# Optimization experiments

Hardware: AMD Instinct MI355X
Metric: run time of the kernel (lower is better)

Reference implementation:

```python
import jax, jax.numpy as jnp
import numpy as np

B, T, D = 2, 1024, 2048
H, KV, DH = 16, 4, 128
REP = H // KV
LAMBDA_INIT = 0.8 - 0.6 * float(np.exp(-0.3 * 1))  # layer_idx=2
ROPE_BASE = 10000.0
GN_EPS = 1e-5


def _rope(x, pos):
    # x: (B, h, T, DH), pos: (T,) int
    inv = 1.0 / (ROPE_BASE ** (jnp.arange(0, DH, 2, dtype=jnp.float32) / DH))
    freqs = pos.astype(jnp.float32)[:, None] * inv[None, :]          # (T, DH/2)
    cos = jnp.cos(freqs)[None, None, :, :].astype(x.dtype)
    sin = jnp.sin(freqs)[None, None, :, :].astype(x.dtype)
    x1, x2 = x[..., ::2], x[..., 1::2]
    o1 = x1 * cos - x2 * sin
    o2 = x1 * sin + x2 * cos
    return jnp.stack([o1, o2], axis=-1).reshape(x.shape)


def setup_inputs() -> dict:
    key = jax.random.key(0)
    ks = jax.random.split(key, 10)
    s = 0.02
    return {
        "x": jax.random.normal(ks[0], (B, T, D), jnp.float32),
        "Wq": jax.random.normal(ks[1], (2 * H * DH, D), jnp.float32) * s,
        "Wk": jax.random.normal(ks[2], (2 * KV * DH, D), jnp.float32) * s,
        "Wv": jax.random.normal(ks[3], (2 * KV * DH, D), jnp.float32) * s,
        "Wo": jax.random.normal(ks[4], (D, 2 * H * DH), jnp.float32) * s,
        "lambda_q1": jax.random.normal(ks[5], (DH,), jnp.float32) * 0.1,
        "lambda_k1": jax.random.normal(ks[6], (DH,), jnp.float32) * 0.1,
        "lambda_q2": jax.random.normal(ks[7], (DH,), jnp.float32) * 0.1,
        "lambda_k2": jax.random.normal(ks[8], (DH,), jnp.float32) * 0.1,
        "gn_weight": jnp.ones((2 * H * DH,), jnp.float32),
        "gn_bias": jnp.zeros((2 * H * DH,), jnp.float32),
        "pos": jnp.arange(T, dtype=jnp.int64 if jax.config.jax_enable_x64 else jnp.int32),
    }


def reference(x, Wq, Wk, Wv, Wo, lambda_q1, lambda_k1, lambda_q2, lambda_k2, gn_weight, gn_bias, pos):
    b, t, _ = x.shape
    # projections
    q = (x @ Wq.T).reshape(b, t, H, 2, DH)        # two query streams per head
    k = (x @ Wk.T).reshape(b, t, KV, 2, DH)       # two key streams per kv-head
    v = (x @ Wv.T).reshape(b, t, KV, 2 * DH)      # single value, 2*Dh per kv-head
    q1 = q[..., 0, :].transpose(0, 2, 1, 3)       # (B,H,T,DH)
    q2 = q[..., 1, :].transpose(0, 2, 1, 3)
    k1 = k[..., 0, :].transpose(0, 2, 1, 3)       # (B,KV,T,DH)
    k2 = k[..., 1, :].transpose(0, 2, 1, 3)
    v = v.transpose(0, 2, 1, 3)                   # (B,KV,T,2DH)
    # RoPE on all Q/K streams
    q1, q2 = _rope(q1, pos), _rope(q2, pos)
    k1, k2 = _rope(k1, pos), _rope(k2, pos)
    # GQA repeat kv heads
    k1 = jnp.repeat(k1, REP, axis=1)
    k2 = jnp.repeat(k2, REP, axis=1)
    vr = jnp.repeat(v, REP, axis=1)               # (B,H,T,2DH)
    scale = DH ** -0.5
    neg = jnp.asarray(-jnp.inf, x.dtype)
    causal = jnp.tril(jnp.ones((t, t), bool))
    s1 = jnp.einsum("bhqd,bhkd->bhqk", q1, k1) * scale
    s2 = jnp.einsum("bhqd,bhkd->bhqk", q2, k2) * scale
    a1 = jax.nn.softmax(jnp.where(causal, s1, neg), axis=-1)
    a2 = jax.nn.softmax(jnp.where(causal, s2, neg), axis=-1)
    lam = (jnp.exp(jnp.sum(lambda_q1 * lambda_k1))
           - jnp.exp(jnp.sum(lambda_q2 * lambda_k2))
           + LAMBDA_INIT)
    attn = a1 - lam * a2
    out = jnp.einsum("bhqk,bhkd->bhqd", attn, vr)  # (B,H,T,2DH)
    # GroupNorm: num_groups=H over 2*H*DH channels == per-head norm over 2*DH
    o = out.transpose(0, 2, 1, 3)                  # (B,T,H,2DH)
    mu = jnp.mean(o, axis=-1, keepdims=True)
    var = jnp.var(o, axis=-1, keepdims=True)
    o = (o - mu) * jax.lax.rsqrt(var + GN_EPS)
    o = o * gn_weight.reshape(H, 2 * DH) + gn_bias.reshape(H, 2 * DH)
    o = o * (1.0 - LAMBDA_INIT)
    o = o.reshape(b, t, 2 * H * DH)
    return o @ Wo.T
```

## Files before the change

kernel.cpp:

```cpp
#include <hip/hip_runtime.h>
#include <hip/hip_bf16.h>

#define BB 2
#define TT 1024
#define DD 2048
#define NH 16
#define NKV 4
#define DHD 128
#define DVV 256

#define LAMBDA_INIT 0.35550906759096927f
#define ONE_MINUS_LI 0.6444909324090307f
#define QSCALE (0.08838834764831845f * 1.4426950408889634f)

typedef __attribute__((ext_vector_type(8))) short bf16x8;
typedef __attribute__((ext_vector_type(4))) float f32x4;

static __device__ __forceinline__ short f2bf_s(float x) {
    __hip_bfloat16 h = __float2bfloat16(x);
    return __builtin_bit_cast(short, h);
}
static __device__ __forceinline__ float bfu2f(unsigned short u) {
    union { float f; unsigned int u32; } x;
    x.u32 = ((unsigned int)u) << 16;
    return x.f;
}

#define GLOAD_LDS16(g, l)                                                      \
    __builtin_amdgcn_global_load_lds(                                          \
        (const __attribute__((address_space(1))) unsigned int*)(g),            \
        (__attribute__((address_space(3))) unsigned int*)(l), 16, 0, 0)

__global__ void cast_bf16(const float* __restrict__ in, __hip_bfloat16* __restrict__ out, int n4) {
    int i = blockIdx.x * blockDim.x + threadIdx.x;
    if (i >= n4) return;
    const float4 v = reinterpret_cast<const float4*>(in)[i];
    union { ushort4 u; __hip_bfloat16 b[4]; } o;
    o.b[0] = __float2bfloat16(v.x);
    o.b[1] = __float2bfloat16(v.y);
    o.b[2] = __float2bfloat16(v.z);
    o.b[3] = __float2bfloat16(v.w);
    reinterpret_cast<ushort4*>(out)[i] = o.u;
}

__global__ __launch_bounds__(256) void gemm128(const __hip_bfloat16* __restrict__ A,
                                               const __hip_bfloat16* __restrict__ Bm,
                                               float* __restrict__ C,
                                               int M, int N, int K) {
    __shared__ ushort As[128 * 32];
    __shared__ ushort Bs[128 * 32];
    const int tid = threadIdx.x;
    const int lane = tid & 63, wid = tid >> 6;
    const int lo = lane & 15, hi = lane >> 4;
    const int wr = wid >> 1, wc = wid & 1;
    const int m0 = blockIdx.y * 128, n0 = blockIdx.x * 128;

    const int srow = tid >> 2;
    const int scol = (tid & 3) << 3;

    const ushort* gA = (const ushort*)A;
    const ushort* gB = (const ushort*)Bm;

    f32x4 acc[4][4];
#pragma unroll
    for (int mi = 0; mi < 4; ++mi)
#pragma unroll
        for (int ni = 0; ni < 4; ++ni) acc[mi][ni] = (f32x4){0.f, 0.f, 0.f, 0.f};

    for (int k0 = 0; k0 < K; k0 += 32) {
        __syncthreads();
#pragma unroll
        for (int i = 0; i < 2; ++i) {
            GLOAD_LDS16(gA + (size_t)(m0 + i * 64 + srow) * K + k0 + scol,
                        &As[(i * 256 + wid * 64) * 8]);
            GLOAD_LDS16(gB + (size_t)(n0 + i * 64 + srow) * K + k0 + scol,
                        &Bs[(i * 256 + wid * 64) * 8]);
        }
        __syncthreads();

        bf16x8 af[4], bfr[4];
#pragma unroll
        for (int mi = 0; mi < 4; ++mi)
            af[mi] = *reinterpret_cast<const bf16x8*>(&As[(wr * 64 + mi * 16 + lo) * 32 + hi * 8]);
#pragma unroll
        for (int ni = 0; ni < 4; ++ni)
            bfr[ni] = *reinterpret_cast<const bf16x8*>(&Bs[(wc * 64 + ni * 16 + lo) * 32 + hi * 8]);
        __builtin_amdgcn_s_setprio(1);
#pragma unroll
        for (int mi = 0; mi < 4; ++mi)
#pragma unroll
            for (int ni = 0; ni < 4; ++ni)
                acc[mi][ni] = __builtin_amdgcn_mfma_f32_16x16x32_bf16(af[mi], bfr[ni], acc[mi][ni], 0, 0, 0);
        __builtin_amdgcn_s_setprio(0);
    }
#pragma unroll
    for (int mi = 0; mi < 4; ++mi)
#pragma unroll
        for (int ni = 0; ni < 4; ++ni)
#pragma unroll
            for (int r = 0; r < 4; ++r)
                C[(size_t)(m0 + wr * 64 + mi * 16 + hi * 4 + r) * N + (n0 + wc * 64 + ni * 16 + lo)] =
                    acc[mi][ni][r];
}

__global__ void rope_qk(const float* __restrict__ in, int stride, int col_base, int nheads, int hshift,
                        const int* __restrict__ pos, __hip_bfloat16* __restrict__ out, float scale) {
    int idx = blockIdx.x * blockDim.x + threadIdx.x;
    int total = BB * TT * nheads * 2 * 64;
    if (idx >= total) return;
    int d2 = idx & 63;
    int rest = idx >> 6;
    int e = rest & 1;
    int rest2 = rest >> 1;
    int head = rest2 & (nheads - 1);
    int bt = rest2 >> hshift;
    int t = bt & (TT - 1);
    int b = bt >> 10;

    const float* src = in + (size_t)bt * stride + col_base + head * 256 + e * 128 + 2 * d2;
    float x1 = src[0], x2 = src[1];
    float inv = expf(-(float)d2 * (2.0f / 128.0f) * 9.210340371976184f);
    float fr = (float)pos[t] * inv;
    float sn, cs;
    sincosf(fr, &sn, &cs);
    float o1 = (x1 * cs - x2 * sn) * scale;
    float o2 = (x1 * sn + x2 * cs) * scale;
    __hip_bfloat16* dst = out + ((((size_t)e * BB + b) * nheads + head) * TT + t) * DHD + 2 * d2;
    dst[0] = __float2bfloat16(o1);
    dst[1] = __float2bfloat16(o2);
}

__global__ void vtrans(const float* __restrict__ in, __hip_bfloat16* __restrict__ out) {
    int idx = blockIdx.x * blockDim.x + threadIdx.x;
    int total = BB * NKV * DVV * TT;
    if (idx >= total) return;
    int t = idx & (TT - 1);
    int rest = idx >> 10;
    int dv = rest & 255;
    int rest2 = rest >> 8;
    int kvi = rest2 & 3;
    int b = rest2 >> 2;
    out[idx] = __float2bfloat16(in[(size_t)(b * TT + t) * 6144 + 5120 + kvi * 256 + dv]);
}

__global__ void lam_k(const float* __restrict__ lq1, const float* __restrict__ lk1,
                      const float* __restrict__ lq2, const float* __restrict__ lk2,
                      float* __restrict__ lam) {
    int l = threadIdx.x;
    float s1 = lq1[l] * lk1[l] + lq1[l + 64] * lk1[l + 64];
    float s2 = lq2[l] * lk2[l] + lq2[l + 64] * lk2[l + 64];
#pragma unroll
    for (int mm = 1; mm < 64; mm <<= 1) {
        s1 += __shfl_xor(s1, mm, 64);
        s2 += __shfl_xor(s2, mm, 64);
    }
    if (l == 0) lam[0] = expf(s1) - expf(s2) + LAMBDA_INIT;
}

__global__ __launch_bounds__(256) void attn_fused(const __hip_bfloat16* __restrict__ qb,
                                                  const __hip_bfloat16* __restrict__ kb,
                                                  const __hip_bfloat16* __restrict__ vtb,
                                                  __hip_bfloat16* __restrict__ Obuf) {
    const int tid = threadIdx.x;
    const int wid = tid >> 6;
    const int lane = tid & 63;
    const int lo = lane & 15, hi = lane >> 4;
    const int qt = (int)gridDim.x - 1 - blockIdx.x;
    const int bh = blockIdx.y;
    const int e = blockIdx.z;
    const int b = bh >> 4, h = bh & 15;
    const int kv = h >> 2;

    const ushort* qp = (const ushort*)qb + (((size_t)e * BB + b) * NH + h) * (size_t)TT * DHD;
    const ushort* kp = (const ushort*)kb + (((size_t)e * BB + b) * NKV + kv) * (size_t)TT * DHD;
    const ushort* vp = (const ushort*)vtb + ((size_t)b * NKV + kv) * (size_t)DVV * TT;

    const int q0 = qt * 64 + wid * 16;

    __shared__ ushort Ks[64 * 128];
    __shared__ ushort Vs[256 * 64];

    bf16x8 qf[4];
#pragma unroll
    for (int kk = 0; kk < 4; ++kk)
        qf[kk] = *reinterpret_cast<const bf16x8*>(qp + (size_t)(q0 + lo) * DHD + kk * 32 + hi * 8);

    f32x4 O[16];
#pragma unroll
    for (int nc = 0; nc < 16; ++nc) O[nc] = (f32x4){0.f, 0.f, 0.f, 0.f};
    float m = -3e38f, l = 0.f;

    const int nkt = qt + 1;
    for (int kt = 0; kt < nkt; ++kt) {
        const int kbase = kt * 64;
#pragma unroll
        for (int p2 = 0; p2 < 4; ++p2) {
            const int idx = p2 * 256 + tid;
            const int row = idx >> 4, c = idx & 15;
            const int cp = c ^ ((row & 3) | ((row >> 1) & 4));
            GLOAD_LDS16(kp + (((size_t)(kbase + row)) << 7) + (cp << 3), &Ks[idx << 3]);
        }
#pragma unroll
        for (int p2 = 0; p2 < 8; ++p2) {
            const int idx = p2 * 256 + tid;
            const int dv = idx >> 3, c = idx & 7;
            const int cp = c ^ (dv & 7);
            GLOAD_LDS16(vp + (size_t)dv * TT + kbase + (cp << 3), &Vs[idx << 3]);
        }
        __syncthreads();

        f32x4 s[4];
#pragma unroll
        for (int n = 0; n < 4; ++n) s[n] = (f32x4){0.f, 0.f, 0.f, 0.f};
        __builtin_amdgcn_s_setprio(1);
#pragma unroll
        for (int n = 0; n < 4; ++n) {
            const int R = ((n >> 1) << 5) + ((lo >> 2) << 3) + ((n & 1) << 2) + (lo & 3);
            const int swz = ((R & 3) | ((R >> 1) & 4)) << 4;
#pragma unroll
            for (int kk = 0; kk < 4; ++kk) {
                bf16x8 kf = *reinterpret_cast<const bf16x8*>(
                    (const char*)Ks + R * 256 + ((kk * 64 + hi * 16) ^ swz));
                s[n] = __builtin_amdgcn_mfma_f32_16x16x32_bf16(kf, qf[kk], s[n], 0, 0, 0);
            }
        }
        __builtin_amdgcn_s_setprio(0);

        if (kt == nkt - 1) {
#pragma unroll
            for (int n = 0; n < 4; ++n) {
                const int kb0 = kbase + ((n >> 1) << 5) + ((n & 1) << 2) + hi * 8;
#pragma unroll
                for (int r = 0; r < 4; ++r)
                    if (kb0 + r > q0 + lo) s[n][r] = -3e38f;
            }
        }
        float tm = s[0][0];
#pragma unroll
        for (int n = 0; n < 4; ++n)
#pragma unroll
            for (int r = 0; r < 4; ++r) tm = fmaxf(tm, s[n][r]);
        tm = fmaxf(tm, __shfl_xor(tm, 16, 64));
        tm = fmaxf(tm, __shfl_xor(tm, 32, 64));
        if (!__all(tm <= m + 11.f)) {
            const float mn = fmaxf(m, tm);
            const float resc = __builtin_amdgcn_exp2f(m - mn);
            m = mn;
            l *= resc;
            float ro[4];
#pragma unroll
            for (int r = 0; r < 4; ++r) ro[r] = __shfl(resc, hi * 4 + r, 64);
#pragma unroll
            for (int nc = 0; nc < 16; ++nc)
#pragma unroll
                for (int r = 0; r < 4; ++r) O[nc][r] *= ro[r];
        }
        float rs = 0.f;
#pragma unroll
        for (int n = 0; n < 4; ++n)
#pragma unroll
            for (int r = 0; r < 4; ++r) {
                const float p = __builtin_amdgcn_exp2f(s[n][r] - m);
                s[n][r] = p;
                rs += p;
            }
        rs += __shfl_xor(rs, 16, 64);
        rs += __shfl_xor(rs, 32, 64);
        l += rs;
        bf16x8 pf[2];
#pragma unroll
        for (int n = 0; n < 4; ++n)
#pragma unroll
            for (int r = 0; r < 4; ++r) pf[n >> 1][(n & 1) * 4 + r] = f2bf_s(s[n][r]);
        __builtin_amdgcn_s_setprio(1);
#pragma unroll
        for (int nc = 0; nc < 16; ++nc) {
            const int vrow = (nc * 16 + lo) * 128;
            const int vswz = (lo & 7) << 4;
#pragma unroll
            for (int ks = 0; ks < 2; ++ks) {
                bf16x8 vf = *reinterpret_cast<const bf16x8*>(
                    (const char*)Vs + vrow + ((ks * 64 + hi * 16) ^ vswz));
                O[nc] = __builtin_amdgcn_mfma_f32_16x16x32_bf16(pf[ks], vf, O[nc], 0, 0, 0);
            }
        }
        __builtin_amdgcn_s_setprio(0);
        __syncthreads();
    }
    const float invl = 1.0f / l;
    float io[4];
#pragma unroll
    for (int r = 0; r < 4; ++r) io[r] = __shfl(invl, hi * 4 + r, 64);
    ushort* op = (ushort*)Obuf + (((size_t)e * BB + b) * NH + h) * (size_t)TT * DVV;
#pragma unroll
    for (int nc = 0; nc < 16; ++nc)
#pragma unroll
        for (int r = 0; r < 4; ++r)
            op[(size_t)(q0 + hi * 4 + r) * DVV + nc * 16 + lo] = (ushort)f2bf_s(O[nc][r] * io[r]);
}

__global__ __launch_bounds__(256) void gn_combine(const __hip_bfloat16* __restrict__ Obuf,
                                                  const float* __restrict__ lamp,
                                                  const float* __restrict__ gw, const float* __restrict__ gb,
                                                  __hip_bfloat16* __restrict__ obf) {
    const int wid = threadIdx.x >> 6, lane = threadIdx.x & 63;
    const int rid = blockIdx.x * 4 + wid;
    const int t = rid & (TT - 1);
    const int h = (rid >> 10) & 15;
    const int b = rid >> 14;
    const float lam = lamp[0];
    const size_t E = (size_t)BB * NH * TT * DVV;
    const ushort* o1p = (const ushort*)Obuf + (size_t)rid * DVV + lane * 4;
    const ushort4 u1 = *reinterpret_cast<const ushort4*>(o1p);
    const ushort4 u2 = *reinterpret_cast<const ushort4*>(o1p + E);
    float val[4];
    val[0] = bfu2f(u1.x) - lam * bfu2f(u2.x);
    val[1] = bfu2f(u1.y) - lam * bfu2f(u2.y);
    val[2] = bfu2f(u1.z) - lam * bfu2f(u2.z);
    val[3] = bfu2f(u1.w) - lam * bfu2f(u2.w);
    float sum = val[0] + val[1] + val[2] + val[3];
    float ss = val[0] * val[0] + val[1] * val[1] + val[2] * val[2] + val[3] * val[3];
#pragma unroll
    for (int mm = 1; mm < 64; mm <<= 1) {
        sum += __shfl_xor(sum, mm, 64);
        ss += __shfl_xor(ss, mm, 64);
    }
    const float mean = sum * (1.0f / 256.0f);
    const float var = ss * (1.0f / 256.0f) - mean * mean;
    const float rs = rsqrtf(var + 1e-5f);
    const int c = h * 256 + lane * 4;
    const float4 gwv = *reinterpret_cast<const float4*>(gw + c);
    const float4 gbv = *reinterpret_cast<const float4*>(gb + c);
    union { ushort4 u; short s[4]; } o;
    o.s[0] = f2bf_s(((val[0] - mean) * rs * gwv.x + gbv.x) * ONE_MINUS_LI);
    o.s[1] = f2bf_s(((val[1] - mean) * rs * gwv.y + gbv.y) * ONE_MINUS_LI);
    o.s[2] = f2bf_s(((val[2] - mean) * rs * gwv.z + gbv.z) * ONE_MINUS_LI);
    o.s[3] = f2bf_s(((val[3] - mean) * rs * gwv.w + gbv.w) * ONE_MINUS_LI);
    const int bt = b * TT + t;
    *reinterpret_cast<ushort4*>((ushort*)obf + (size_t)bt * 4096 + c) = o.u;
}

extern "C" void kernel_launch(void* const* d_in, const int* in_sizes, int n_in,
                              void* d_out, int out_size, void* d_ws, size_t ws_size,
                              hipStream_t stream) {
    const float* x = (const float*)d_in[0];
    const float* Wq = (const float*)d_in[1];
    const float* Wk = (const float*)d_in[2];
    const float* Wv = (const float*)d_in[3];
    const float* Wo = (const float*)d_in[4];
    const float* lq1 = (const float*)d_in[5];
    const float* lk1 = (const float*)d_in[6];
    const float* lq2 = (const float*)d_in[7];
    const float* lk2 = (const float*)d_in[8];
    const float* gw = (const float*)d_in[9];
    const float* gb = (const float*)d_in[10];
    const int* pos = (const int*)d_in[11];

    char* ws = (char*)d_ws;
    const size_t oXB = 0;
    const size_t oWQKV = 8388608;
    const size_t oWO = 33554432;
    const size_t oQKVF = 50331648;
    const size_t oOB = 50331648;
    const size_t oLAM = 83886080;
    const size_t oQB = 100663296;
    const size_t oKB = 117440512;
    const size_t oVT = 121634816;
    const size_t oON = 125829120;

    auto bfp = [&](size_t off) { return (__hip_bfloat16*)(ws + off); };
    auto fp = [&](size_t off) { return (float*)(ws + off); };

    int n;
    n = BB * TT * DD / 4;
    cast_bf16<<<dim3((n + 255) / 256), 256, 0, stream>>>(x, bfp(oXB), n);
    n = 4096 * 2048 / 4;
    cast_bf16<<<dim3((n + 255) / 256), 256, 0, stream>>>(Wq, bfp(oWQKV), n);
    n = 1024 * 2048 / 4;
    cast_bf16<<<dim3((n + 255) / 256), 256, 0, stream>>>(Wk, bfp(oWQKV + (size_t)4096 * 2048 * 2), n);
    cast_bf16<<<dim3((n + 255) / 256), 256, 0, stream>>>(Wv, bfp(oWQKV + (size_t)5120 * 2048 * 2), n);
    n = 2048 * 4096 / 4;
    cast_bf16<<<dim3((n + 255) / 256), 256, 0, stream>>>(Wo, bfp(oWO), n);

    gemm128<<<dim3(6144 / 128, 2048 / 128), 256, 0, stream>>>(bfp(oXB), bfp(oWQKV), fp(oQKVF), 2048, 6144, 2048);

    n = BB * TT * NH * 2 * 64;
    rope_qk<<<dim3((n + 255) / 256), 256, 0, stream>>>(fp(oQKVF), 6144, 0, NH, 4, pos, bfp(oQB), QSCALE);
    n = BB * TT * NKV * 2 * 64;
    rope_qk<<<dim3((n + 255) / 256), 256, 0, stream>>>(fp(oQKVF), 6144, 4096, NKV, 2, pos, bfp(oKB), 1.0f);
    n = BB * NKV * DVV * TT;
    vtrans<<<dim3((n + 255) / 256), 256, 0, stream>>>(fp(oQKVF), bfp(oVT));

    lam_k<<<dim3(1), 64, 0, stream>>>(lq1, lk1, lq2, lk2, fp(oLAM));

    attn_fused<<<dim3(TT / 64, BB * NH, 2), 256, 0, stream>>>(bfp(oQB), bfp(oKB), bfp(oVT), bfp(oOB));

    gn_combine<<<dim3(BB * NH * TT / 4), 256, 0, stream>>>(bfp(oOB), fp(oLAM), gw, gb, bfp(oON));

    gemm128<<<dim3(2048 / 128, 2048 / 128), 256, 0, stream>>>(bfp(oON), bfp(oWO), (float*)d_out, 2048, 2048, 4096);
}
```

Before: 484.4 us.

## Double-buffer GEMM LDS, split-K output projection, tile V transpose through LDS

The GEMM now keeps two LDS buffers, issuing the next K-tile's global-to-LDS loads before computing on the current one, so each iteration needs one barrier instead of two. The output projection is split along K into two slices written to a scratch partial buffer, then summed by a new addf4 kernel; this doubles the block count for a grid that otherwise fills the CUs only once, at the cost of extra partial-sum traffic and a launch. The V transpose now goes through a padded LDS tile so both the reads and the writes to global memory are coalesced. The s_setprio hints are removed.

```diff
diff --git a/kernel.cpp b/kernel.cpp
--- a/kernel.cpp
+++ b/kernel.cpp
@@ -43,23 +43,35 @@
     reinterpret_cast<ushort4*>(out)[i] = o.u;
 }
 
-__global__ __launch_bounds__(256) void gemm128(const __hip_bfloat16* __restrict__ A,
-                                               const __hip_bfloat16* __restrict__ Bm,
-                                               float* __restrict__ C,
-                                               int M, int N, int K) {
-    __shared__ ushort As[128 * 32];
-    __shared__ ushort Bs[128 * 32];
+__global__ __launch_bounds__(256) void gemm128_db(const __hip_bfloat16* __restrict__ A,
+                                                  const __hip_bfloat16* __restrict__ Bm,
+                                                  float* __restrict__ C,
+                                                  int M, int N, int sK, int kLen) {
+    __shared__ ushort As[2][128 * 32];
+    __shared__ ushort Bs[2][128 * 32];
     const int tid = threadIdx.x;
     const int lane = tid & 63, wid = tid >> 6;
     const int lo = lane & 15, hi = lane >> 4;
     const int wr = wid >> 1, wc = wid & 1;
     const int m0 = blockIdx.y * 128, n0 = blockIdx.x * 128;
-
-    const int srow = tid >> 2;
-    const int scol = (tid & 3) << 3;
+    const int kOff = blockIdx.z * kLen;
 
     const ushort* gA = (const ushort*)A;
     const ushort* gB = (const ushort*)Bm;
+    C += (size_t)blockIdx.z * M * N;
+
+    const int c0row = tid >> 2;
+    const int c0col = (tid & 3) << 3;
+
+    auto STAGE = [&](int buf, int kg) {
+#pragma unroll
+        for (int q = 0; q < 2; ++q) {
+            const int row = q * 64 + c0row;
+            const int idx = q * 256 + tid;
+            GLOAD_LDS16(gA + (size_t)(m0 + row) * sK + kg + c0col, &As[buf][idx << 3]);
+            GLOAD_LDS16(gB + (size_t)(n0 + row) * sK + kg + c0col, &Bs[buf][idx << 3]);
+        }
+    };
 
     f32x4 acc[4][4];
 #pragma unroll
@@ -67,31 +79,25 @@
 #pragma unroll
         for (int ni = 0; ni < 4; ++ni) acc[mi][ni] = (f32x4){0.f, 0.f, 0.f, 0.f};
 
-    for (int k0 = 0; k0 < K; k0 += 32) {
+    STAGE(0, kOff);
+    const int nt = kLen >> 5;
+    for (int t = 0; t < nt; ++t) {
         __syncthreads();
-#pragma unroll
-        for (int i = 0; i < 2; ++i) {
-            GLOAD_LDS16(gA + (size_t)(m0 + i * 64 + srow) * K + k0 + scol,
-                        &As[(i * 256 + wid * 64) * 8]);
-            GLOAD_LDS16(gB + (size_t)(n0 + i * 64 + srow) * K + k0 + scol,
-                        &Bs[(i * 256 + wid * 64) * 8]);
-        }
-        __syncthreads();
-
+        if (t + 1 < nt) STAGE((t + 1) & 1, kOff + ((t + 1) << 5));
+        const ushort* as = &As[t & 1][0];
+        const ushort* bs = &Bs[t & 1][0];
         bf16x8 af[4], bfr[4];
 #pragma unroll
         for (int mi = 0; mi < 4; ++mi)
-            af[mi] = *reinterpret_cast<const bf16x8*>(&As[(wr * 64 + mi * 16 + lo) * 32 + hi * 8]);
+            af[mi] = *reinterpret_cast<const bf16x8*>(&as[(wr * 64 + mi * 16 + lo) * 32 + hi * 8]);
 #pragma unroll
         for (int ni = 0; ni < 4; ++ni)
-            bfr[ni] = *reinterpret_cast<const bf16x8*>(&Bs[(wc * 64 + ni * 16 + lo) * 32 + hi * 8]);
-        __builtin_amdgcn_s_setprio(1);
+            bfr[ni] = *reinterpret_cast<const bf16x8*>(&bs[(wc * 64 + ni * 16 + lo) * 32 + hi * 8]);
 #pragma unroll
         for (int mi = 0; mi < 4; ++mi)
 #pragma unroll
             for (int ni = 0; ni < 4; ++ni)
                 acc[mi][ni] = __builtin_amdgcn_mfma_f32_16x16x32_bf16(af[mi], bfr[ni], acc[mi][ni], 0, 0, 0);
-        __builtin_amdgcn_s_setprio(0);
     }
 #pragma unroll
     for (int mi = 0; mi < 4; ++mi)
@@ -101,6 +107,16 @@
             for (int r = 0; r < 4; ++r)
                 C[(size_t)(m0 + wr * 64 + mi * 16 + hi * 4 + r) * N + (n0 + wc * 64 + ni * 16 + lo)] =
                     acc[mi][ni][r];
+}
+
+__global__ void addf4(const float* __restrict__ p, float* __restrict__ out, int n4) {
+    int i = blockIdx.x * blockDim.x + threadIdx.x;
+    if (i >= n4) return;
+    const float4 a = reinterpret_cast<const float4*>(p)[i];
+    const float4 b = reinterpret_cast<const float4*>(p)[i + n4];
+    float4 o;
+    o.x = a.x + b.x; o.y = a.y + b.y; o.z = a.z + b.z; o.w = a.w + b.w;
+    reinterpret_cast<float4*>(out)[i] = o;
 }
 
 __global__ void rope_qk(const float* __restrict__ in, int stride, int col_base, int nheads, int hshift,
@@ -130,17 +146,26 @@
     dst[1] = __float2bfloat16(o2);
 }
 
-__global__ void vtrans(const float* __restrict__ in, __hip_bfloat16* __restrict__ out) {
-    int idx = blockIdx.x * blockDim.x + threadIdx.x;
-    int total = BB * NKV * DVV * TT;
-    if (idx >= total) return;
-    int t = idx & (TT - 1);
-    int rest = idx >> 10;
-    int dv = rest & 255;
-    int rest2 = rest >> 8;
-    int kvi = rest2 & 3;
-    int b = rest2 >> 2;
-    out[idx] = __float2bfloat16(in[(size_t)(b * TT + t) * 6144 + 5120 + kvi * 256 + dv]);
+__global__ __launch_bounds__(256) void vtrans(const float* __restrict__ in, __hip_bfloat16* __restrict__ out) {
+    __shared__ float tle[64][65];
+    const int t0 = blockIdx.x * 64;
+    const int z = blockIdx.y;
+    const int dv0 = (z & 3) * 64;
+    const int kvi = (z >> 2) & 3;
+    const int b = z >> 4;
+    const int tid = threadIdx.x;
+    const int rt = tid >> 6, ct = tid & 63;
+#pragma unroll
+    for (int p = 0; p < 16; ++p) {
+        const int ti = p * 4 + rt;
+        tle[ti][ct] = in[(size_t)(b * TT + t0 + ti) * 6144 + 5120 + kvi * 256 + dv0 + ct];
+    }
+    __syncthreads();
+#pragma unroll
+    for (int p = 0; p < 16; ++p) {
+        const int dv = p * 4 + rt;
+        out[((size_t)(b * NKV + kvi) * DVV + dv0 + dv) * TT + t0 + ct] = __float2bfloat16(tle[ct][dv]);
+    }
 }
 
 __global__ void lam_k(const float* __restrict__ lq1, const float* __restrict__ lk1,
@@ -362,6 +387,7 @@
     const size_t oWO = 33554432;
     const size_t oQKVF = 50331648;
     const size_t oOB = 50331648;
+    const size_t oPK = 50331648;
     const size_t oLAM = 83886080;
     const size_t oQB = 100663296;
     const size_t oKB = 117440512;
@@ -382,14 +408,14 @@
     n = 2048 * 4096 / 4;
     cast_bf16<<<dim3((n + 255) / 256), 256, 0, stream>>>(Wo, bfp(oWO), n);
 
-    gemm128<<<dim3(6144 / 128, 2048 / 128), 256, 0, stream>>>(bfp(oXB), bfp(oWQKV), fp(oQKVF), 2048, 6144, 2048);
+    gemm128_db<<<dim3(6144 / 128, 2048 / 128, 1), 256, 0, stream>>>(
+        bfp(oXB), bfp(oWQKV), fp(oQKVF), 2048, 6144, 2048, 2048);
 
     n = BB * TT * NH * 2 * 64;
     rope_qk<<<dim3((n + 255) / 256), 256, 0, stream>>>(fp(oQKVF), 6144, 0, NH, 4, pos, bfp(oQB), QSCALE);
     n = BB * TT * NKV * 2 * 64;
     rope_qk<<<dim3((n + 255) / 256), 256, 0, stream>>>(fp(oQKVF), 6144, 4096, NKV, 2, pos, bfp(oKB), 1.0f);
-    n = BB * NKV * DVV * TT;
-    vtrans<<<dim3((n + 255) / 256), 256, 0, stream>>>(fp(oQKVF), bfp(oVT));
+    vtrans<<<dim3(TT / 64, BB * NKV * 4), 256, 0, stream>>>(fp(oQKVF), bfp(oVT));
 
     lam_k<<<dim3(1), 64, 0, stream>>>(lq1, lk1, lq2, lk2, fp(oLAM));
 
@@ -397,5 +423,8 @@
 
     gn_combine<<<dim3(BB * NH * TT / 4), 256, 0, stream>>>(bfp(oOB), fp(oLAM), gw, gb, bfp(oON));
 
-    gemm128<<<dim3(2048 / 128, 2048 / 128), 256, 0, stream>>>(bfp(oON), bfp(oWO), (float*)d_out, 2048, 2048, 4096);
-}
+    gemm128_db<<<dim3(2048 / 128, 2048 / 128, 2), 256, 0, stream>>>(
+        bfp(oON), bfp(oWO), fp(oPK), 2048, 2048, 4096, 2048);
+    n = 2048 * 2048 / 4;
+    addf4<<<dim3((n + 255) / 256), 256, 0, stream>>>(fp(oPK), (float*)d_out, n);
+}
```

Result: faster. 438.3 us (-9.5%).
